# Kernel optimization log

Measured on AMD Instinct MI355X. Metric: run time of the kernel, lower is better.

## Reference

```python
import jax, jax.numpy as jnp
import numpy as np

LN_EPS = 1e-3  # keras LayerNormalization default epsilon


def setup_inputs() -> dict:
    key = jax.random.key(0)
    ks = jax.random.split(key, 6)
    B, S, D, H, K = 4, 4096, 1024, 16, 64
    scale = 1.0 / np.sqrt(D)
    return {
        "x": jax.random.normal(ks[0], (B, S, D), jnp.float32),
        "Wq": jax.random.normal(ks[1], (D, H, K), jnp.float32) * scale,
        "bq": jnp.zeros((H, K), jnp.float32),
        "Wk": jax.random.normal(ks[2], (D, H, K), jnp.float32) * scale,
        "bk": jnp.zeros((H, K), jnp.float32),
        "Wv": jax.random.normal(ks[3], (D, H, K), jnp.float32) * scale,
        "bv": jnp.zeros((H, K), jnp.float32),
        "Wo": jax.random.normal(ks[4], (H, K, D), jnp.float32) * scale,
        "bo": jnp.zeros((D,), jnp.float32),
        "gamma": jnp.ones((D,), jnp.float32),
        "beta": jnp.zeros((D,), jnp.float32),
        "num_window": 8,
    }


def reference(x, Wq, bq, Wk, bk, Wv, bv, Wo, bo, gamma, beta, num_window):
    B, S, D = x.shape
    H, K = Wq.shape[1], Wq.shape[2]
    Sw = S // num_window
    # Block-diagonal (windowed) attention: reshape seq into windows instead of a Python loop.
    xw = x.reshape(B, num_window, Sw, D)  # [B, W, Sw, D]
    q = jnp.einsum('bwsd,dhk->bwshk', xw, Wq) + bq
    k = jnp.einsum('bwsd,dhk->bwshk', xw, Wk) + bk
    v = jnp.einsum('bwsd,dhk->bwshk', xw, Wv) + bv
    scores = jnp.einsum('bwqhk,bwshk->bwhqs', q, k) / jnp.sqrt(jnp.asarray(K, x.dtype))
    attn = jax.nn.softmax(scores, axis=-1)  # [B, W, H, Sw, Sw]
    ctx = jnp.einsum('bwhqs,bwshk->bwqhk', attn, v)
    attn_out = (jnp.einsum('bwqhk,hkd->bwqd', ctx, Wo) + bo).reshape(B, S, D)
    # residual + layernorm (keras eps=1e-3)
    y = x + attn_out
    mu = jnp.mean(y, axis=-1, keepdims=True)
    var = jnp.mean(jnp.square(y - mu), axis=-1, keepdims=True)
    return (y - mu) * jax.lax.rsqrt(var + LN_EPS) * gamma + beta
```

## Files before the change

### kernel.cpp

```cpp
#include <hip/hip_runtime.h>

typedef __bf16 bf16_t;
typedef __bf16 bf16x4 __attribute__((ext_vector_type(4)));
typedef __bf16 bf16x8 __attribute__((ext_vector_type(8)));
typedef float f32x4 __attribute__((ext_vector_type(4)));
typedef float f32x16 __attribute__((ext_vector_type(16)));

#define MFMA16(a, b, c) __builtin_amdgcn_mfma_f32_16x16x32_bf16((a), (b), (c), 0, 0, 0)
#define MFMA32(a, b, c) __builtin_amdgcn_mfma_f32_32x32x16_bf16((a), (b), (c), 0, 0, 0)

__device__ __forceinline__ void gl_lds16(const bf16_t* g, bf16_t* l) {
  __builtin_amdgcn_global_load_lds(
      (const __attribute__((address_space(1))) void*)g,
      (__attribute__((address_space(3))) void*)l, 16, 0, 0);
}

__global__ __launch_bounds__(256) void cast_x_kernel(const float* __restrict__ x,
                                                     bf16_t* __restrict__ xb) {
  size_t i = (size_t)blockIdx.x * 256 + threadIdx.x;
  float4 v = ((const float4*)x)[i];
  bf16x4 o = {(bf16_t)v.x, (bf16_t)v.y, (bf16_t)v.z, (bf16_t)v.w};
  ((bf16x4*)xb)[i] = o;
}

__global__ __launch_bounds__(256) void transpose_w_kernel(
    const float* __restrict__ Wq, const float* __restrict__ Wk,
    const float* __restrict__ Wv, const float* __restrict__ Wo,
    bf16_t* __restrict__ Wt, bf16_t* __restrict__ WoT) {
  __shared__ bf16_t T[64 * 68];
  const int z = blockIdx.z;
  const float* src = (z == 0) ? Wq : (z == 1) ? Wk : (z == 2) ? Wv : Wo;
  bf16_t* dst = (z < 3) ? (Wt + (size_t)z * 1024 * 1024) : WoT;
  const int tr = blockIdx.y * 64;
  const int tc = blockIdx.x * 64;
  const int tid = threadIdx.x;
#pragma unroll
  for (int it = 0; it < 4; ++it) {
    int t = tid + it * 256;
    int row = t >> 4, c4 = t & 15;
    float4 v = *(const float4*)&src[(size_t)(tr + row) * 1024 + tc + c4 * 4];
    bf16x4 o = {(bf16_t)v.x, (bf16_t)v.y, (bf16_t)v.z, (bf16_t)v.w};
    *(bf16x4*)&T[row * 68 + c4 * 4] = o;
  }
  __syncthreads();
#pragma unroll
  for (int it = 0; it < 2; ++it) {
    int t = tid + it * 256;
    int n = t >> 3, d8 = t & 7;
    bf16x8 o;
#pragma unroll
    for (int j = 0; j < 8; ++j) o[j] = T[(d8 * 8 + j) * 68 + n];
    *(bf16x8*)&dst[(size_t)(tc + n) * 1024 + tr + d8 * 8] = o;
  }
}

__global__ __launch_bounds__(256) void gemm_qkv_kernel(
    const bf16_t* __restrict__ A, const bf16_t* __restrict__ Bt,
    const float* __restrict__ bq, const float* __restrict__ bk,
    const float* __restrict__ bv, bf16_t* __restrict__ C) {
  __shared__ bf16_t As[128 * 64];
  __shared__ bf16_t Bs[128 * 64];
  const int tid = threadIdx.x;
  const int bm = blockIdx.y, bn = blockIdx.x;
  const int lane = tid & 63;
  const int l31 = lane & 31, lh = lane >> 5;
  const int wv = tid >> 6;
  const int wm = (wv & 1) * 64, wn = (wv >> 1) * 64;

  f32x16 acc[2][2];
#pragma unroll
  for (int i = 0; i < 2; ++i)
#pragma unroll
    for (int j = 0; j < 2; ++j)
#pragma unroll
      for (int e = 0; e < 16; ++e) acc[i][j][e] = 0.f;

  const bf16_t* Abase = A + (size_t)(bm * 128) * 1024;
  const bf16_t* Bbase = Bt + (size_t)(bn * 128) * 1024;

  for (int kt = 0; kt < 16; ++kt) {
    const int k0 = kt * 64;
#pragma unroll
    for (int i = 0; i < 4; ++i) {
      int t = tid + i * 256;
      int row = t >> 3;
      int g = (t & 7) ^ (row & 7);
      gl_lds16(Abase + (size_t)row * 1024 + k0 + g * 8, &As[t * 8]);
      gl_lds16(Bbase + (size_t)row * 1024 + k0 + g * 8, &Bs[t * 8]);
    }
    __syncthreads();
#pragma unroll
    for (int ks = 0; ks < 4; ++ks) {
      bf16x8 af[2], bfr[2];
#pragma unroll
      for (int mi = 0; mi < 2; ++mi) {
        int r = wm + mi * 32 + l31;
        af[mi] = *(const bf16x8*)&As[r * 64 + (((ks * 2 + lh) ^ (r & 7)) << 3)];
      }
#pragma unroll
      for (int ni = 0; ni < 2; ++ni) {
        int r = wn + ni * 32 + l31;
        bfr[ni] = *(const bf16x8*)&Bs[r * 64 + (((ks * 2 + lh) ^ (r & 7)) << 3)];
      }
#pragma unroll
      for (int mi = 0; mi < 2; ++mi)
#pragma unroll
        for (int ni = 0; ni < 2; ++ni)
          acc[mi][ni] = MFMA32(af[mi], bfr[ni], acc[mi][ni]);
    }
    __syncthreads();
  }

#pragma unroll
  for (int ni = 0; ni < 2; ++ni) {
    int col = bn * 128 + wn + ni * 32 + l31;
    float bias, scale;
    if (col < 1024) {
      bias = bq[col];
      scale = 0.125f;
    } else if (col < 2048) {
      bias = bk[col - 1024];
      scale = 1.f;
    } else {
      bias = bv[col - 2048];
      scale = 1.f;
    }
#pragma unroll
    for (int mi = 0; mi < 2; ++mi) {
      int rowb = bm * 128 + wm + mi * 32 + 4 * lh;
#pragma unroll
      for (int reg = 0; reg < 16; ++reg) {
        int row = rowb + (reg & 3) + 8 * (reg >> 2);
        C[(size_t)row * 3072 + col] = (bf16_t)((acc[mi][ni][reg] + bias) * scale);
      }
    }
  }
}

__global__ __launch_bounds__(256) void attn_kernel(
    const bf16_t* __restrict__ QKV, bf16_t* __restrict__ Ctx) {
  __shared__ bf16_t Ks[64 * 64];
  __shared__ bf16_t Vs[64 * 64];
  __shared__ bf16_t Pb[4][16 * 64];

  const int tid = threadIdx.x;
  const int wv = tid >> 6, quad = (tid >> 4) & 3, l15 = tid & 15;
  const int hid = blockIdx.x, qb = blockIdx.y;
  const int b = hid >> 7, w = (hid >> 4) & 7, h = hid & 15;
  const int rowW = b * 4096 + w * 512;
  const int qbase = qb * 128 + wv * 32;

  bf16x8 qf[2][2];
#pragma unroll
  for (int qt = 0; qt < 2; ++qt) {
    int rowQ = rowW + qbase + qt * 16 + l15;
#pragma unroll
    for (int kh = 0; kh < 2; ++kh)
      qf[qt][kh] = *(const bf16x8*)&QKV[(size_t)rowQ * 3072 + h * 64 + kh * 32 + quad * 8];
  }

  const bf16_t* Kb = QKV + (size_t)rowW * 3072 + 1024 + h * 64;
  const bf16_t* Vg = QKV + (size_t)rowW * 3072 + 2048 + h * 64;

  float lp[2] = {0.f, 0.f};
  f32x4 Oa[2][4];
  f32x4 zero = {0.f, 0.f, 0.f, 0.f};
#pragma unroll
  for (int qt = 0; qt < 2; ++qt)
#pragma unroll
    for (int dt = 0; dt < 4; ++dt) Oa[qt][dt] = zero;

  const int vrow = tid >> 2;
  const int vseg = tid & 3;

  for (int kt = 0; kt < 8; ++kt) {
#pragma unroll
    for (int i = 0; i < 2; ++i) {
      int t = tid + i * 256;
      int row = t >> 3;
      int g = (t & 7) ^ (row & 7);
      gl_lds16(Kb + (size_t)(kt * 64 + row) * 3072 + g * 8, &Ks[t * 8]);
    }
    {
      const bf16_t* src = Vg + (size_t)(kt * 64 + vrow) * 3072 + vseg * 16;
      bf16x8 v0 = *(const bf16x8*)&src[0];
      bf16x8 v1 = *(const bf16x8*)&src[8];
      int sg = vrow >> 3, sr = vrow & 7;
#pragma unroll
      for (int j = 0; j < 8; ++j) {
        int d0 = vseg * 16 + j;
        Vs[d0 * 64 + ((sg ^ (d0 & 7)) << 3) + sr] = v0[j];
        int d1 = vseg * 16 + 8 + j;
        Vs[d1 * 64 + ((sg ^ (d1 & 7)) << 3) + sr] = v1[j];
      }
    }
    __syncthreads();

    bf16x8 kf[4][2], vf[2][4];
#pragma unroll
    for (int jt = 0; jt < 4; ++jt) {
      int key = jt * 16 + l15;
#pragma unroll
      for (int kh = 0; kh < 2; ++kh)
        kf[jt][kh] = *(const bf16x8*)&Ks[key * 64 + (((kh * 4 + quad) ^ (key & 7)) << 3)];
    }
#pragma unroll
    for (int kh = 0; kh < 2; ++kh)
#pragma unroll
      for (int dt = 0; dt < 4; ++dt) {
        int d = dt * 16 + l15;
        vf[kh][dt] = *(const bf16x8*)&Vs[d * 64 + (((kh * 4 + quad) ^ (d & 7)) << 3)];
      }

#pragma unroll
    for (int qt = 0; qt < 2; ++qt) {
      f32x4 st[4];
#pragma unroll
      for (int jt = 0; jt < 4; ++jt) {
        f32x4 a = zero;
#pragma unroll
        for (int kh = 0; kh < 2; ++kh) a = MFMA16(kf[jt][kh], qf[qt][kh], a);
        st[jt] = a;
      }
      float ls = 0.f;
#pragma unroll
      for (int jt = 0; jt < 4; ++jt)
#pragma unroll
        for (int r = 0; r < 4; ++r) {
          float p = __expf(st[jt][r]);
          st[jt][r] = p;
          ls += p;
        }
      lp[qt] += ls;
#pragma unroll
      for (int jt = 0; jt < 4; ++jt) {
        bf16x4 pk = {(bf16_t)st[jt][0], (bf16_t)st[jt][1],
                     (bf16_t)st[jt][2], (bf16_t)st[jt][3]};
        int gs = (jt * 2 + (quad >> 1)) ^ (l15 & 7);
        *(bf16x4*)&Pb[wv][l15 * 64 + gs * 8 + (quad & 1) * 4] = pk;
      }
#pragma unroll
      for (int kh = 0; kh < 2; ++kh) {
        bf16x8 pf = *(const bf16x8*)&Pb[wv][l15 * 64 + (((kh * 4 + quad) ^ (l15 & 7)) << 3)];
#pragma unroll
        for (int dt = 0; dt < 4; ++dt) Oa[qt][dt] = MFMA16(pf, vf[kh][dt], Oa[qt][dt]);
      }
    }
    __syncthreads();
  }

#pragma unroll
  for (int qt = 0; qt < 2; ++qt) {
    float t = lp[qt];
    t += __shfl_xor(t, 16, 64);
    t += __shfl_xor(t, 32, 64);
    float inv_l = 1.0f / t;
    float inv[4];
#pragma unroll
    for (int r = 0; r < 4; ++r) inv[r] = __shfl(inv_l, quad * 4 + r, 64);
#pragma unroll
    for (int dt = 0; dt < 4; ++dt)
#pragma unroll
      for (int r = 0; r < 4; ++r) {
        int orow = rowW + qbase + qt * 16 + quad * 4 + r;
        Ctx[(size_t)orow * 1024 + h * 64 + dt * 16 + l15] = (bf16_t)(Oa[qt][dt][r] * inv[r]);
      }
  }
}

__global__ __launch_bounds__(256) void gemm_proj_kernel(
    const bf16_t* __restrict__ A, const bf16_t* __restrict__ Bt,
    const float* __restrict__ bo, const float* __restrict__ x,
    bf16_t* __restrict__ Yb) {
  __shared__ bf16_t As[128 * 64];
  __shared__ bf16_t Bs[128 * 64];
  const int tid = threadIdx.x;
  const int bm = blockIdx.y, bn = blockIdx.x;
  const int lane = tid & 63;
  const int l31 = lane & 31, lh = lane >> 5;
  const int wv = tid >> 6;
  const int wm = (wv & 1) * 64, wn = (wv >> 1) * 64;

  f32x16 acc[2][2];
#pragma unroll
  for (int i = 0; i < 2; ++i)
#pragma unroll
    for (int j = 0; j < 2; ++j)
#pragma unroll
      for (int e = 0; e < 16; ++e) acc[i][j][e] = 0.f;

  const bf16_t* Abase = A + (size_t)(bm * 128) * 1024;
  const bf16_t* Bbase = Bt + (size_t)(bn * 128) * 1024;

  for (int kt = 0; kt < 16; ++kt) {
    const int k0 = kt * 64;
#pragma unroll
    for (int i = 0; i < 4; ++i) {
      int t = tid + i * 256;
      int row = t >> 3;
      int g = (t & 7) ^ (row & 7);
      gl_lds16(Abase + (size_t)row * 1024 + k0 + g * 8, &As[t * 8]);
      gl_lds16(Bbase + (size_t)row * 1024 + k0 + g * 8, &Bs[t * 8]);
    }
    __syncthreads();
#pragma unroll
    for (int ks = 0; ks < 4; ++ks) {
      bf16x8 af[2], bfr[2];
#pragma unroll
      for (int mi = 0; mi < 2; ++mi) {
        int r = wm + mi * 32 + l31;
        af[mi] = *(const bf16x8*)&As[r * 64 + (((ks * 2 + lh) ^ (r & 7)) << 3)];
      }
#pragma unroll
      for (int ni = 0; ni < 2; ++ni) {
        int r = wn + ni * 32 + l31;
        bfr[ni] = *(const bf16x8*)&Bs[r * 64 + (((ks * 2 + lh) ^ (r & 7)) << 3)];
      }
#pragma unroll
      for (int mi = 0; mi < 2; ++mi)
#pragma unroll
        for (int ni = 0; ni < 2; ++ni)
          acc[mi][ni] = MFMA32(af[mi], bfr[ni], acc[mi][ni]);
    }
    __syncthreads();
  }

#pragma unroll
  for (int ni = 0; ni < 2; ++ni) {
    int col = bn * 128 + wn + ni * 32 + l31;
    float bias = bo[col];
#pragma unroll
    for (int mi = 0; mi < 2; ++mi) {
      int rowb = bm * 128 + wm + mi * 32 + 4 * lh;
#pragma unroll
      for (int reg = 0; reg < 16; ++reg) {
        int row = rowb + (reg & 3) + 8 * (reg >> 2);
        size_t idx = (size_t)row * 1024 + col;
        Yb[idx] = (bf16_t)(acc[mi][ni][reg] + bias + x[idx]);
      }
    }
  }
}

__global__ __launch_bounds__(256) void ln_kernel(const bf16_t* __restrict__ Yb,
                                                 float* __restrict__ Y,
                                                 const float* __restrict__ gamma,
                                                 const float* __restrict__ beta) {
  const int row = blockIdx.x, tid = threadIdx.x;
  bf16x4 yb = ((const bf16x4*)(Yb + (size_t)row * 1024))[tid];
  float y0 = (float)yb[0], y1 = (float)yb[1], y2 = (float)yb[2], y3 = (float)yb[3];
  float s = y0 + y1 + y2 + y3;
  float s2 = y0 * y0 + y1 * y1 + y2 * y2 + y3 * y3;
#pragma unroll
  for (int off = 1; off < 64; off <<= 1) {
    s += __shfl_xor(s, off, 64);
    s2 += __shfl_xor(s2, off, 64);
  }
  __shared__ float red[8];
  int wv = tid >> 6;
  if ((tid & 63) == 0) {
    red[wv] = s;
    red[4 + wv] = s2;
  }
  __syncthreads();
  s = red[0] + red[1] + red[2] + red[3];
  s2 = red[4] + red[5] + red[6] + red[7];
  float mean = s * (1.0f / 1024.0f);
  float var = s2 * (1.0f / 1024.0f) - mean * mean;
  float rs = rsqrtf(var + 1e-3f);
  float4 g = ((const float4*)gamma)[tid];
  float4 bb = ((const float4*)beta)[tid];
  float4 o;
  o.x = (y0 - mean) * rs * g.x + bb.x;
  o.y = (y1 - mean) * rs * g.y + bb.y;
  o.z = (y2 - mean) * rs * g.z + bb.z;
  o.w = (y3 - mean) * rs * g.w + bb.w;
  ((float4*)(Y + (size_t)row * 1024))[tid] = o;
}

extern "C" void kernel_launch(void* const* d_in, const int* in_sizes, int n_in,
                              void* d_out, int out_size, void* d_ws, size_t ws_size,
                              hipStream_t stream) {
  const float* x = (const float*)d_in[0];
  const float* Wq = (const float*)d_in[1];
  const float* bq = (const float*)d_in[2];
  const float* Wk = (const float*)d_in[3];
  const float* bk = (const float*)d_in[4];
  const float* Wv = (const float*)d_in[5];
  const float* bv = (const float*)d_in[6];
  const float* Wo = (const float*)d_in[7];
  const float* bo = (const float*)d_in[8];
  const float* gamma = (const float*)d_in[9];
  const float* beta = (const float*)d_in[10];
  float* Y = (float*)d_out;

  char* ws = (char*)d_ws;
  bf16_t* xb = (bf16_t*)(ws);
  bf16_t* Wt = (bf16_t*)(ws + 33554432);
  bf16_t* WoT = (bf16_t*)(ws + 39845888);
  bf16_t* QKVb = (bf16_t*)(ws + 41943040);
  bf16_t* Ctx = (bf16_t*)(ws + 142606336);
  bf16_t* Yb = (bf16_t*)(ws + 176160768);

  cast_x_kernel<<<16384, 256, 0, stream>>>(x, xb);
  transpose_w_kernel<<<dim3(16, 16, 4), 256, 0, stream>>>(Wq, Wk, Wv, Wo, Wt, WoT);
  gemm_qkv_kernel<<<dim3(24, 128), 256, 0, stream>>>(xb, Wt, bq, bk, bv, QKVb);
  attn_kernel<<<dim3(512, 4), 256, 0, stream>>>(QKVb, Ctx);
  gemm_proj_kernel<<<dim3(8, 128), 256, 0, stream>>>(Ctx, WoT, bo, x, Yb);
  ln_kernel<<<16384, 256, 0, stream>>>(Yb, Y, gamma, beta);
}
```

Baseline: 411.4 us.

## Double-buffer K/V tiles in attention kernel and prefetch next tile

The attention kernel now keeps two LDS buffers for K and V. It issues the global loads for the next key tile before computing on the current one, and writes the transposed V into the other buffer after the MFMA work, so only one barrier per iteration remains. The V transpose swizzle also changes to fold in higher bits of d, which should cut LDS bank conflicts. K and V fragments are read from LDS inside the MFMA loops instead of being preloaded into registers. The trade-off is twice the LDS and the prefetched V values held in registers across the compute phase.

```diff
diff --git a/kernel.cpp b/kernel.cpp
--- a/kernel.cpp
+++ b/kernel.cpp
@@ -139,8 +139,8 @@
 
 __global__ __launch_bounds__(256) void attn_kernel(
     const bf16_t* __restrict__ QKV, bf16_t* __restrict__ Ctx) {
-  __shared__ bf16_t Ks[64 * 64];
-  __shared__ bf16_t Vs[64 * 64];
+  __shared__ bf16_t Ks[2][64 * 64];
+  __shared__ bf16_t Vs[2][64 * 64];
   __shared__ bf16_t Pb[4][16 * 64];
 
   const int tid = threadIdx.x;
@@ -172,45 +172,47 @@
 
   const int vrow = tid >> 2;
   const int vseg = tid & 3;
+  const int sg = vrow >> 3, sr = vrow & 7;
+
+#pragma unroll
+  for (int i = 0; i < 2; ++i) {
+    int t = tid + i * 256;
+    int row = t >> 3;
+    int g = (t & 7) ^ (row & 7);
+    gl_lds16(Kb + (size_t)row * 3072 + g * 8, &Ks[0][t * 8]);
+  }
+  {
+    const bf16_t* src = Vg + (size_t)vrow * 3072 + vseg * 16;
+    bf16x8 v0 = *(const bf16x8*)&src[0];
+    bf16x8 v1 = *(const bf16x8*)&src[8];
+#pragma unroll
+    for (int j = 0; j < 8; ++j) {
+      int d0 = vseg * 16 + j;
+      int f0 = (d0 ^ (d0 >> 3)) & 7;
+      Vs[0][d0 * 64 + ((sg ^ f0) << 3) + sr] = v0[j];
+      int d1 = d0 + 8;
+      int f1 = (d1 ^ (d1 >> 3)) & 7;
+      Vs[0][d1 * 64 + ((sg ^ f1) << 3) + sr] = v1[j];
+    }
+  }
 
   for (int kt = 0; kt < 8; ++kt) {
-#pragma unroll
-    for (int i = 0; i < 2; ++i) {
-      int t = tid + i * 256;
-      int row = t >> 3;
-      int g = (t & 7) ^ (row & 7);
-      gl_lds16(Kb + (size_t)(kt * 64 + row) * 3072 + g * 8, &Ks[t * 8]);
-    }
-    {
-      const bf16_t* src = Vg + (size_t)(kt * 64 + vrow) * 3072 + vseg * 16;
-      bf16x8 v0 = *(const bf16x8*)&src[0];
-      bf16x8 v1 = *(const bf16x8*)&src[8];
-      int sg = vrow >> 3, sr = vrow & 7;
-#pragma unroll
-      for (int j = 0; j < 8; ++j) {
-        int d0 = vseg * 16 + j;
-        Vs[d0 * 64 + ((sg ^ (d0 & 7)) << 3) + sr] = v0[j];
-        int d1 = vseg * 16 + 8 + j;
-        Vs[d1 * 64 + ((sg ^ (d1 & 7)) << 3) + sr] = v1[j];
-      }
-    }
+    const int cur = kt & 1, nxt = cur ^ 1;
     __syncthreads();
 
-    bf16x8 kf[4][2], vf[2][4];
-#pragma unroll
-    for (int jt = 0; jt < 4; ++jt) {
-      int key = jt * 16 + l15;
-#pragma unroll
-      for (int kh = 0; kh < 2; ++kh)
-        kf[jt][kh] = *(const bf16x8*)&Ks[key * 64 + (((kh * 4 + quad) ^ (key & 7)) << 3)];
-    }
-#pragma unroll
-    for (int kh = 0; kh < 2; ++kh)
-#pragma unroll
-      for (int dt = 0; dt < 4; ++dt) {
-        int d = dt * 16 + l15;
-        vf[kh][dt] = *(const bf16x8*)&Vs[d * 64 + (((kh * 4 + quad) ^ (d & 7)) << 3)];
-      }
+    bf16x8 v0n, v1n;
+    if (kt < 7) {
+#pragma unroll
+      for (int i = 0; i < 2; ++i) {
+        int t = tid + i * 256;
+        int row = t >> 3;
+        int g = (t & 7) ^ (row & 7);
+        gl_lds16(Kb + (size_t)((kt + 1) * 64 + row) * 3072 + g * 8, &Ks[nxt][t * 8]);
+      }
+      const bf16_t* src = Vg + (size_t)((kt + 1) * 64 + vrow) * 3072 + vseg * 16;
+      v0n = *(const bf16x8*)&src[0];
+      v1n = *(const bf16x8*)&src[8];
+    }
 
 #pragma unroll
     for (int qt = 0; qt < 2; ++qt) {
@@ -219,7 +221,11 @@
       for (int jt = 0; jt < 4; ++jt) {
         f32x4 a = zero;
 #pragma unroll
-        for (int kh = 0; kh < 2; ++kh) a = MFMA16(kf[jt][kh], qf[qt][kh], a);
+        for (int kh = 0; kh < 2; ++kh) {
+          int key = jt * 16 + l15;
+          bf16x8 kf = *(const bf16x8*)&Ks[cur][key * 64 + (((kh * 4 + quad) ^ (key & 7)) << 3)];
+          a = MFMA16(kf, qf[qt][kh], a);
+        }
         st[jt] = a;
       }
       float ls = 0.f;
@@ -243,10 +249,26 @@
       for (int kh = 0; kh < 2; ++kh) {
         bf16x8 pf = *(const bf16x8*)&Pb[wv][l15 * 64 + (((kh * 4 + quad) ^ (l15 & 7)) << 3)];
 #pragma unroll
-        for (int dt = 0; dt < 4; ++dt) Oa[qt][dt] = MFMA16(pf, vf[kh][dt], Oa[qt][dt]);
-      }
-    }
-    __syncthreads();
+        for (int dt = 0; dt < 4; ++dt) {
+          int d = dt * 16 + l15;
+          int fd = (d ^ (d >> 3)) & 7;
+          bf16x8 vf = *(const bf16x8*)&Vs[cur][d * 64 + (((kh * 4 + quad) ^ fd) << 3)];
+          Oa[qt][dt] = MFMA16(pf, vf, Oa[qt][dt]);
+        }
+      }
+    }
+
+    if (kt < 7) {
+#pragma unroll
+      for (int j = 0; j < 8; ++j) {
+        int d0 = vseg * 16 + j;
+        int f0 = (d0 ^ (d0 >> 3)) & 7;
+        Vs[nxt][d0 * 64 + ((sg ^ f0) << 3) + sr] = v0n[j];
+        int d1 = d0 + 8;
+        int f1 = (d1 ^ (d1 >> 3)) & 7;
+        Vs[nxt][d1 * 64 + ((sg ^ f1) << 3) + sr] = v1n[j];
+      }
+    }
   }
 
 #pragma unroll
```

After: 417.7 us. About the same (+1.5%).
